# Kernel optimization log

Hardware: AMD Instinct MI355X
Metric: run time of the kernel (lower is better)

Reference implementation:

```python
import jax, jax.numpy as jnp
import numpy as np
import math

# ShiftedL2Loss constants derived from init kwargs
SAMPLE_RATE = 48000
ALPHA = 100.0
MAX_DIST = 1.5
DIST_SAMPLES = int(SAMPLE_RATE * MAX_DIST / 340)  # 211
T_WIN = 2 ** int(math.floor(math.log(DIST_SAMPLES, 2)))  # t = 128
S_SHIFTS = T_WIN * 2 + 1                                  # S = 257
T_BIG = T_WIN + S_SHIFTS - 1                              # T = 384
DT = T_WIN                                                # dT = t


def _blackman_window(M):
    # torch.blackman_window(M, periodic=False)
    n = jnp.arange(M, dtype=jnp.float32)
    denom = jnp.float32(M - 1)
    return (0.42 - 0.5 * jnp.cos(2.0 * jnp.pi * n / denom)
            + 0.08 * jnp.cos(4.0 * jnp.pi * n / denom))


def setup_inputs() -> dict:
    key = jax.random.key(0)
    k1, k2 = jax.random.split(key)
    B, C, L = 4, 8, 15104  # L = 118 * 128 -> exact tiling
    data = jax.random.normal(k1, (B, C, L), dtype=jnp.float32)
    target = jax.random.normal(k2, (B, C, L), dtype=jnp.float32)
    return {"data": data, "target": target}


def reference(data, target):
    t, S = T_WIN, S_SHIFTS
    w = ALPHA * (1.0 - _blackman_window(S))  # (S,)

    # flatten to (BC, L)
    x = data.reshape(-1, data.shape[-1])
    r = target.reshape(-1, target.shape[-1])
    L = x.shape[-1]
    N = (L - t) // DT + 1
    Ltrim = (N - 1) * DT + t
    x = x[:, :Ltrim]
    r = r[:, :Ltrim]

    # magnitude normalization on the center region
    d = x[:, t:-t]
    rc = r[:, t:-t]
    d = d - jnp.mean(d, axis=1, keepdims=True)
    rc = rc - jnp.mean(rc, axis=1, keepdims=True)
    mag_x = jnp.sqrt(jnp.mean(d ** 2, axis=1, keepdims=True))
    mag_r = jnp.sqrt(jnp.mean(rc ** 2, axis=1, keepdims=True))
    mag_min = jnp.minimum(mag_x, mag_r)
    mag_norm = jnp.sqrt(mag_min * mag_r) + 0.001  # (BC, 1)
    x = x / mag_norm
    r = r / mag_norm

    # zero-pad reference by t on both sides
    r_pad = jnp.pad(r, ((0, 0), (t, t)))  # (BC, Ltrim + 2t)

    # non-overlapping predicted windows: (BC, N, t)
    xw = x.reshape(-1, N, t)

    # shifted reference windows: (BC, N, S, t)
    starts = (jnp.arange(N) * DT)[:, None, None]
    idx = starts + jnp.arange(S)[None, :, None] + jnp.arange(t)[None, None, :]
    yw = r_pad[:, idx]  # gather -> (BC, N, S, t)

    # per-shift MSE over the window: (BC, N, S)
    mse = jnp.mean((xw[:, :, None, :] - yw) ** 2, axis=-1)

    # shift-weighted penalty, min over shifts, mean over everything
    loss = (mse + 1.0) * (w[None, None, :] + 1.0) - 1.0
    loss = jnp.amin(loss, axis=-1)  # (BC, N)
    return jnp.mean(loss).reshape(1)
```

## Files before the change

### kernel.cpp

```cpp
#include <hip/hip_runtime.h>
#include <math.h>

#define ROWS 32
#define LROW 15104
#define TWIN 128
#define SSH  257
#define NWIN 118
#define TRIM 14848
#define NW   (ROWS * NWIN)
#define NBLK (NW / 4)
#define SEGS 8
#define SEGLEN (TRIM / SEGS)
#define NSEG4 (SEGLEN / 4)


__global__ __launch_bounds__(256) void stats_partial(
        const float* __restrict__ data,
        const float* __restrict__ target,
        float4* __restrict__ partials) {
    int blk = blockIdx.x;
    int row = blk >> 3;
    int seg = blk & 7;
    int tid = threadIdx.x;

    const float4* x4 = (const float4*)(data   + row * LROW + TWIN + seg * SEGLEN);
    const float4* r4 = (const float4*)(target + row * LROW + TWIN + seg * SEGLEN);
    float sd = 0.f, sd2 = 0.f, sr = 0.f, sr2 = 0.f;
    for (int i = tid; i < NSEG4; i += 256) {
        float4 a = x4[i], b = r4[i];
        sd  += a.x + a.y + a.z + a.w;
        sd2 += a.x*a.x + a.y*a.y + a.z*a.z + a.w*a.w;
        sr  += b.x + b.y + b.z + b.w;
        sr2 += b.x*b.x + b.y*b.y + b.z*b.z + b.w*b.w;
    }
    __shared__ float sh[4][256];
    sh[0][tid] = sd; sh[1][tid] = sd2; sh[2][tid] = sr; sh[3][tid] = sr2;
    __syncthreads();
    for (int off = 128; off > 0; off >>= 1) {
        if (tid < off) {
            sh[0][tid] += sh[0][tid + off];
            sh[1][tid] += sh[1][tid + off];
            sh[2][tid] += sh[2][tid + off];
            sh[3][tid] += sh[3][tid + off];
        }
        __syncthreads();
    }
    if (tid == 0)
        partials[blk] = make_float4(sh[0][0], sh[1][0], sh[2][0], sh[3][0]);
}

__global__ __launch_bounds__(256) void loss_kernel(
        const float* __restrict__ data,
        const float* __restrict__ target,
        const float4* __restrict__ partials,
        float* __restrict__ blocksums) {
    int tid  = threadIdx.x;
    int wave = tid >> 6;
    int lane = tid & 63;
    int widx = blockIdx.x * 4 + wave;
    int row  = widx / NWIN;
    int n    = widx % NWIN;

    float scale;
    {
        const float4* pr = partials + row * SEGS;
        float sd = 0.f, sd2 = 0.f, sr = 0.f, sr2 = 0.f;
        #pragma unroll
        for (int i = 0; i < SEGS; ++i) {
            float4 p = pr[i];
            sd += p.x; sd2 += p.y; sr += p.z; sr2 += p.w;
        }
        const float inv = 1.0f / (float)TRIM;
        float md = sd * inv, mr = sr * inv;
        float vx = fmaxf(sd2 * inv - md * md, 0.f);
        float vr = fmaxf(sr2 * inv - mr * mr, 0.f);
        float mag_x = sqrtf(vx), mag_r = sqrtf(vr);
        float mag_min = fminf(mag_x, mag_r);
        scale = 1.0f / (sqrtf(mag_min * mag_r) + 0.001f);
    }

    __shared__ float xs[4][TWIN];
    __shared__ float ys[4][3 * TWIN];

    const float* xr = data   + row * LROW + n * TWIN;
    const float* rr = target + row * LROW;
    int base = n * TWIN;

    {
        float2 v = *(const float2*)(xr + 2 * lane);
        xs[wave][2 * lane]     = v.x * scale;
        xs[wave][2 * lane + 1] = v.y * scale;
    }
    for (int j = lane; j < 96; j += 64) {
        int g0 = base + 4 * j - TWIN;
        float4 v = make_float4(0.f, 0.f, 0.f, 0.f);
        if (g0 >= 0 && g0 < LROW) v = *(const float4*)(rr + g0);
        *(float4*)&ys[wave][4 * j] =
            make_float4(v.x * scale, v.y * scale, v.z * scale, v.w * scale);
    }

    float sx, part;
    {
        float xa = xs[wave][lane], xb = xs[wave][lane + 64];
        float ya = ys[wave][256 + lane], yb = ys[wave][320 + lane];
        float d1 = xa - ya, d2 = xb - yb;
        part = d1 * d1 + d2 * d2;
        sx   = xa * xa + xb * xb;
        #pragma unroll
        for (int off = 32; off > 0; off >>= 1) {
            part += __shfl_xor(part, off, 64);
            sx   += __shfl_xor(sx,   off, 64);
        }
    }

    const float4* xs4 = (const float4*)xs[wave];
    const float4* ys4 = (const float4*)ys[wave];

    float4 yv0 = ys4[lane];
    float yf0 = yv0.x, yf1 = yv0.y, yf2 = yv0.z;
    float c0 = 0.f, c1 = 0.f, c2 = 0.f, c3 = 0.f;
    float q = 0.f;

    #pragma unroll
    for (int kb = 0; kb < 32; ++kb) {
        float4 xv  = xs4[kb];
        float4 yv1 = ys4[lane + kb + 1];
        c0 += xv.x*yv0.x + xv.y*yv0.y + xv.z*yv0.z + xv.w*yv0.w;
        c1 += xv.x*yv0.y + xv.y*yv0.z + xv.z*yv0.w + xv.w*yv1.x;
        c2 += xv.x*yv0.z + xv.y*yv0.w + xv.z*yv1.x + xv.w*yv1.y;
        c3 += xv.x*yv0.w + xv.y*yv1.x + xv.z*yv1.y + xv.w*yv1.z;
        q  += yv0.x*yv0.x + yv0.y*yv0.y + yv0.z*yv0.z + yv0.w*yv0.w;
        yv0 = yv1;
    }
    float sy0 = q;
    float sy1 = sy0 - yf0*yf0 + yv0.x*yv0.x;
    float sy2 = sy1 - yf1*yf1 + yv0.y*yv0.y;
    float sy3 = sy2 - yf2*yf2 + yv0.z*yv0.z;

    const float inv = 1.0f / (float)TWIN;
    int   s0  = lane * 4;
    float lmin = 1e30f;
    {
        float mse, ph, cp, bw, w;
        mse = (sx - 2.f*c0 + sy0) * inv;
        ph  = (float)(s0 + 0) * (float)(M_PI / 128.0);
        cp  = __cosf(ph); bw = 0.42f - 0.5f*cp + 0.08f*(2.f*cp*cp - 1.f);
        w   = 100.f * (1.f - bw);
        lmin = fminf(lmin, (mse + 1.f) * (w + 1.f) - 1.f);
        mse = (sx - 2.f*c1 + sy1) * inv;
        ph  = (float)(s0 + 1) * (float)(M_PI / 128.0);
        cp  = __cosf(ph); bw = 0.42f - 0.5f*cp + 0.08f*(2.f*cp*cp - 1.f);
        w   = 100.f * (1.f - bw);
        lmin = fminf(lmin, (mse + 1.f) * (w + 1.f) - 1.f);
        mse = (sx - 2.f*c2 + sy2) * inv;
        ph  = (float)(s0 + 2) * (float)(M_PI / 128.0);
        cp  = __cosf(ph); bw = 0.42f - 0.5f*cp + 0.08f*(2.f*cp*cp - 1.f);
        w   = 100.f * (1.f - bw);
        lmin = fminf(lmin, (mse + 1.f) * (w + 1.f) - 1.f);
        mse = (sx - 2.f*c3 + sy3) * inv;
        ph  = (float)(s0 + 3) * (float)(M_PI / 128.0);
        cp  = __cosf(ph); bw = 0.42f - 0.5f*cp + 0.08f*(2.f*cp*cp - 1.f);
        w   = 100.f * (1.f - bw);
        lmin = fminf(lmin, (mse + 1.f) * (w + 1.f) - 1.f);
    }

    {
        float mse256 = part * inv;
        float l256 = (mse256 + 1.f) * 101.f - 1.f;
        lmin = fminf(lmin, l256);
    }
    #pragma unroll
    for (int off = 32; off > 0; off >>= 1)
        lmin = fminf(lmin, __shfl_xor(lmin, off, 64));

    __shared__ float wl[4];
    if (lane == 0) wl[wave] = lmin;
    __syncthreads();
    if (tid == 0) {
        blocksums[blockIdx.x] =
            ((wl[0] + wl[1]) + (wl[2] + wl[3]));
    }
}

__global__ __launch_bounds__(256) void finish_kernel(
        const float* __restrict__ blocksums,
        float* __restrict__ out) {
    int tid = threadIdx.x;
    float s = 0.f;
    for (int i = tid; i < NBLK; i += 256) s += blocksums[i];
    __shared__ float sh[256];
    sh[tid] = s;
    __syncthreads();
    for (int off = 128; off > 0; off >>= 1) {
        if (tid < off) sh[tid] += sh[tid + off];
        __syncthreads();
    }
    if (tid == 0) out[0] = sh[0] / (float)NW;
}

extern "C" void kernel_launch(void* const* d_in, const int* in_sizes, int n_in,
                              void* d_out, int out_size, void* d_ws, size_t ws_size,
                              hipStream_t stream) {
    const float* data   = (const float*)d_in[0];
    const float* target = (const float*)d_in[1];
    float4* partials  = (float4*)d_ws;
    float*  blocksums = (float*)((char*)d_ws + 8192);

    stats_partial<<<ROWS * SEGS, 256, 0, stream>>>(data, target, partials);
    loss_kernel<<<NBLK, 256, 0, stream>>>(data, target, partials, blocksums);
    finish_kernel<<<1, 256, 0, stream>>>(blocksums, (float*)d_out);
}
```

Before: 19.54 us.

## Fuse row statistics into loss kernel with 8-window blocks sharing reference panel

Removes the separate statistics kernel: each block recomputes the full-row mean and energy sums before scaling its windows. Blocks now process eight consecutive windows with a shared reference panel, and a block index swizzle spreads work across dies. This saves a kernel launch and the dependency between launches, at the cost of every block redundantly reading the whole row (mostly from L2).

Measured after the change: 18.39 us. -5.9%, faster.

```diff
diff --git a/kernel.cpp b/kernel.cpp
--- a/kernel.cpp
+++ b/kernel.cpp
@@ -4,70 +4,62 @@
 #define ROWS 32
 #define LROW 15104
 #define TWIN 128
-#define SSH  257
 #define NWIN 118
 #define TRIM 14848
 #define NW   (ROWS * NWIN)
-#define NBLK (NW / 4)
-#define SEGS 8
-#define SEGLEN (TRIM / SEGS)
-#define NSEG4 (SEGLEN / 4)
-
-
-__global__ __launch_bounds__(256) void stats_partial(
+#define WPB  8
+#define BPR  15
+#define NBLK (ROWS * BPR)
+#define XPAN (WPB * TWIN)
+#define YPAN ((WPB + 3) * TWIN)
+
+__global__ __launch_bounds__(512) void loss_fused(
         const float* __restrict__ data,
         const float* __restrict__ target,
-        float4* __restrict__ partials) {
-    int blk = blockIdx.x;
-    int row = blk >> 3;
-    int seg = blk & 7;
-    int tid = threadIdx.x;
-
-    const float4* x4 = (const float4*)(data   + row * LROW + TWIN + seg * SEGLEN);
-    const float4* r4 = (const float4*)(target + row * LROW + TWIN + seg * SEGLEN);
-    float sd = 0.f, sd2 = 0.f, sr = 0.f, sr2 = 0.f;
-    for (int i = tid; i < NSEG4; i += 256) {
-        float4 a = x4[i], b = r4[i];
-        sd  += a.x + a.y + a.z + a.w;
-        sd2 += a.x*a.x + a.y*a.y + a.z*a.z + a.w*a.w;
-        sr  += b.x + b.y + b.z + b.w;
-        sr2 += b.x*b.x + b.y*b.y + b.z*b.z + b.w*b.w;
-    }
-    __shared__ float sh[4][256];
-    sh[0][tid] = sd; sh[1][tid] = sd2; sh[2][tid] = sr; sh[3][tid] = sr2;
-    __syncthreads();
-    for (int off = 128; off > 0; off >>= 1) {
-        if (tid < off) {
-            sh[0][tid] += sh[0][tid + off];
-            sh[1][tid] += sh[1][tid + off];
-            sh[2][tid] += sh[2][tid + off];
-            sh[3][tid] += sh[3][tid + off];
-        }
-        __syncthreads();
-    }
-    if (tid == 0)
-        partials[blk] = make_float4(sh[0][0], sh[1][0], sh[2][0], sh[3][0]);
-}
-
-__global__ __launch_bounds__(256) void loss_kernel(
-        const float* __restrict__ data,
-        const float* __restrict__ target,
-        const float4* __restrict__ partials,
         float* __restrict__ blocksums) {
+    int b0 = blockIdx.x;
+    int b  = (b0 & 7) * (NBLK / 8) + (b0 >> 3);
+    int row = b / BPR;
+    int n0  = (b % BPR) * WPB;
     int tid  = threadIdx.x;
     int wave = tid >> 6;
     int lane = tid & 63;
-    int widx = blockIdx.x * 4 + wave;
-    int row  = widx / NWIN;
-    int n    = widx % NWIN;
-
-    float scale;
+
+    __shared__ float xs[XPAN];
+    __shared__ float ys[YPAN];
+    __shared__ float4 wsum[8];
+    __shared__ float s_scale;
+    __shared__ float wl[8];
+
+    const float* xrow = data   + row * LROW;
+    const float* rrow = target + row * LROW;
+
     {
-        const float4* pr = partials + row * SEGS;
+        const float4* x4 = (const float4*)(xrow + TWIN);
+        const float4* r4 = (const float4*)(rrow + TWIN);
         float sd = 0.f, sd2 = 0.f, sr = 0.f, sr2 = 0.f;
-        #pragma unroll
-        for (int i = 0; i < SEGS; ++i) {
-            float4 p = pr[i];
+        for (int i = tid; i < TRIM / 4; i += 512) {
+            float4 a = x4[i], bv = r4[i];
+            sd  += a.x + a.y + a.z + a.w;
+            sd2 += a.x*a.x + a.y*a.y + a.z*a.z + a.w*a.w;
+            sr  += bv.x + bv.y + bv.z + bv.w;
+            sr2 += bv.x*bv.x + bv.y*bv.y + bv.z*bv.z + bv.w*bv.w;
+        }
+        #pragma unroll
+        for (int off = 32; off > 0; off >>= 1) {
+            sd  += __shfl_xor(sd,  off, 64);
+            sd2 += __shfl_xor(sd2, off, 64);
+            sr  += __shfl_xor(sr,  off, 64);
+            sr2 += __shfl_xor(sr2, off, 64);
+        }
+        if (lane == 0) wsum[wave] = make_float4(sd, sd2, sr, sr2);
+    }
+    __syncthreads();
+    if (tid == 0) {
+        float sd = 0.f, sd2 = 0.f, sr = 0.f, sr2 = 0.f;
+        #pragma unroll
+        for (int i = 0; i < 8; ++i) {
+            float4 p = wsum[i];
             sd += p.x; sd2 += p.y; sr += p.z; sr2 += p.w;
         }
         const float inv = 1.0f / (float)TRIM;
@@ -76,109 +68,113 @@
         float vr = fmaxf(sr2 * inv - mr * mr, 0.f);
         float mag_x = sqrtf(vx), mag_r = sqrtf(vr);
         float mag_min = fminf(mag_x, mag_r);
-        scale = 1.0f / (sqrtf(mag_min * mag_r) + 0.001f);
-    }
-
-    __shared__ float xs[4][TWIN];
-    __shared__ float ys[4][3 * TWIN];
-
-    const float* xr = data   + row * LROW + n * TWIN;
-    const float* rr = target + row * LROW;
-    int base = n * TWIN;
-
-    {
-        float2 v = *(const float2*)(xr + 2 * lane);
-        xs[wave][2 * lane]     = v.x * scale;
-        xs[wave][2 * lane + 1] = v.y * scale;
-    }
-    for (int j = lane; j < 96; j += 64) {
-        int g0 = base + 4 * j - TWIN;
+        s_scale = 1.0f / (sqrtf(mag_min * mag_r) + 0.001f);
+    }
+    __syncthreads();
+    float scale = s_scale;
+
+    for (int j = tid; j < XPAN / 4; j += 512) {
+        int g = n0 * TWIN + 4 * j;
         float4 v = make_float4(0.f, 0.f, 0.f, 0.f);
-        if (g0 >= 0 && g0 < LROW) v = *(const float4*)(rr + g0);
-        *(float4*)&ys[wave][4 * j] =
+        if (g < LROW) v = *(const float4*)(xrow + g);
+        *(float4*)&xs[4 * j] =
             make_float4(v.x * scale, v.y * scale, v.z * scale, v.w * scale);
     }
-
-    float sx, part;
-    {
-        float xa = xs[wave][lane], xb = xs[wave][lane + 64];
-        float ya = ys[wave][256 + lane], yb = ys[wave][320 + lane];
-        float d1 = xa - ya, d2 = xb - yb;
-        part = d1 * d1 + d2 * d2;
-        sx   = xa * xa + xb * xb;
-        #pragma unroll
-        for (int off = 32; off > 0; off >>= 1) {
-            part += __shfl_xor(part, off, 64);
-            sx   += __shfl_xor(sx,   off, 64);
-        }
-    }
-
-    const float4* xs4 = (const float4*)xs[wave];
-    const float4* ys4 = (const float4*)ys[wave];
-
-    float4 yv0 = ys4[lane];
-    float yf0 = yv0.x, yf1 = yv0.y, yf2 = yv0.z;
-    float c0 = 0.f, c1 = 0.f, c2 = 0.f, c3 = 0.f;
-    float q = 0.f;
-
-    #pragma unroll
-    for (int kb = 0; kb < 32; ++kb) {
-        float4 xv  = xs4[kb];
-        float4 yv1 = ys4[lane + kb + 1];
-        c0 += xv.x*yv0.x + xv.y*yv0.y + xv.z*yv0.z + xv.w*yv0.w;
-        c1 += xv.x*yv0.y + xv.y*yv0.z + xv.z*yv0.w + xv.w*yv1.x;
-        c2 += xv.x*yv0.z + xv.y*yv0.w + xv.z*yv1.x + xv.w*yv1.y;
-        c3 += xv.x*yv0.w + xv.y*yv1.x + xv.z*yv1.y + xv.w*yv1.z;
-        q  += yv0.x*yv0.x + yv0.y*yv0.y + yv0.z*yv0.z + yv0.w*yv0.w;
-        yv0 = yv1;
-    }
-    float sy0 = q;
-    float sy1 = sy0 - yf0*yf0 + yv0.x*yv0.x;
-    float sy2 = sy1 - yf1*yf1 + yv0.y*yv0.y;
-    float sy3 = sy2 - yf2*yf2 + yv0.z*yv0.z;
-
-    const float inv = 1.0f / (float)TWIN;
-    int   s0  = lane * 4;
-    float lmin = 1e30f;
-    {
-        float mse, ph, cp, bw, w;
-        mse = (sx - 2.f*c0 + sy0) * inv;
-        ph  = (float)(s0 + 0) * (float)(M_PI / 128.0);
-        cp  = __cosf(ph); bw = 0.42f - 0.5f*cp + 0.08f*(2.f*cp*cp - 1.f);
-        w   = 100.f * (1.f - bw);
-        lmin = fminf(lmin, (mse + 1.f) * (w + 1.f) - 1.f);
-        mse = (sx - 2.f*c1 + sy1) * inv;
-        ph  = (float)(s0 + 1) * (float)(M_PI / 128.0);
-        cp  = __cosf(ph); bw = 0.42f - 0.5f*cp + 0.08f*(2.f*cp*cp - 1.f);
-        w   = 100.f * (1.f - bw);
-        lmin = fminf(lmin, (mse + 1.f) * (w + 1.f) - 1.f);
-        mse = (sx - 2.f*c2 + sy2) * inv;
-        ph  = (float)(s0 + 2) * (float)(M_PI / 128.0);
-        cp  = __cosf(ph); bw = 0.42f - 0.5f*cp + 0.08f*(2.f*cp*cp - 1.f);
-        w   = 100.f * (1.f - bw);
-        lmin = fminf(lmin, (mse + 1.f) * (w + 1.f) - 1.f);
-        mse = (sx - 2.f*c3 + sy3) * inv;
-        ph  = (float)(s0 + 3) * (float)(M_PI / 128.0);
-        cp  = __cosf(ph); bw = 0.42f - 0.5f*cp + 0.08f*(2.f*cp*cp - 1.f);
-        w   = 100.f * (1.f - bw);
-        lmin = fminf(lmin, (mse + 1.f) * (w + 1.f) - 1.f);
-    }
-
-    {
-        float mse256 = part * inv;
-        float l256 = (mse256 + 1.f) * 101.f - 1.f;
-        lmin = fminf(lmin, l256);
-    }
-    #pragma unroll
-    for (int off = 32; off > 0; off >>= 1)
-        lmin = fminf(lmin, __shfl_xor(lmin, off, 64));
-
-    __shared__ float wl[4];
+    for (int j = tid; j < YPAN / 4; j += 512) {
+        int g = (n0 - 1) * TWIN + 4 * j;
+        float4 v = make_float4(0.f, 0.f, 0.f, 0.f);
+        if (g >= 0 && g < LROW) v = *(const float4*)(rrow + g);
+        *(float4*)&ys[4 * j] =
+            make_float4(v.x * scale, v.y * scale, v.z * scale, v.w * scale);
+    }
+    __syncthreads();
+
+    int n = n0 + wave;
+    float lmin = 0.f;
+    if (n < NWIN) {
+        const float* xw = xs + wave * TWIN;
+        const float* yw = ys + wave * TWIN;
+
+        float sx, part;
+        {
+            float xa = xw[lane], xb = xw[lane + 64];
+            float ya = yw[256 + lane], yb = yw[320 + lane];
+            float d1 = xa - ya, d2 = xb - yb;
+            part = d1 * d1 + d2 * d2;
+            sx   = xa * xa + xb * xb;
+            #pragma unroll
+            for (int off = 32; off > 0; off >>= 1) {
+                part += __shfl_xor(part, off, 64);
+                sx   += __shfl_xor(sx,   off, 64);
+            }
+        }
+
+        const float4* xs4 = (const float4*)xw;
+        const float4* ys4 = (const float4*)yw;
+
+        float4 yv0 = ys4[lane];
+        float yf0 = yv0.x, yf1 = yv0.y, yf2 = yv0.z;
+        float c0 = 0.f, c1 = 0.f, c2 = 0.f, c3 = 0.f;
+        float q = 0.f;
+
+        #pragma unroll
+        for (int kb = 0; kb < 32; ++kb) {
+            float4 xv  = xs4[kb];
+            float4 yv1 = ys4[lane + kb + 1];
+            c0 += xv.x*yv0.x + xv.y*yv0.y + xv.z*yv0.z + xv.w*yv0.w;
+            c1 += xv.x*yv0.y + xv.y*yv0.z + xv.z*yv0.w + xv.w*yv1.x;
+            c2 += xv.x*yv0.z + xv.y*yv0.w + xv.z*yv1.x + xv.w*yv1.y;
+            c3 += xv.x*yv0.w + xv.y*yv1.x + xv.z*yv1.y + xv.w*yv1.z;
+            q  += yv0.x*yv0.x + yv0.y*yv0.y + yv0.z*yv0.z + yv0.w*yv0.w;
+            yv0 = yv1;
+        }
+        float sy0 = q;
+        float sy1 = sy0 - yf0*yf0 + yv0.x*yv0.x;
+        float sy2 = sy1 - yf1*yf1 + yv0.y*yv0.y;
+        float sy3 = sy2 - yf2*yf2 + yv0.z*yv0.z;
+
+        const float inv = 1.0f / (float)TWIN;
+        int   s0  = lane * 4;
+        lmin = 1e30f;
+        {
+            float mse, ph, cp, bw, w;
+            mse = (sx - 2.f*c0 + sy0) * inv;
+            ph  = (float)(s0 + 0) * (float)(M_PI / 128.0);
+            cp  = __cosf(ph); bw = 0.42f - 0.5f*cp + 0.08f*(2.f*cp*cp - 1.f);
+            w   = 100.f * (1.f - bw);
+            lmin = fminf(lmin, (mse + 1.f) * (w + 1.f) - 1.f);
+            mse = (sx - 2.f*c1 + sy1) * inv;
+            ph  = (float)(s0 + 1) * (float)(M_PI / 128.0);
+            cp  = __cosf(ph); bw = 0.42f - 0.5f*cp + 0.08f*(2.f*cp*cp - 1.f);
+            w   = 100.f * (1.f - bw);
+            lmin = fminf(lmin, (mse + 1.f) * (w + 1.f) - 1.f);
+            mse = (sx - 2.f*c2 + sy2) * inv;
+            ph  = (float)(s0 + 2) * (float)(M_PI / 128.0);
+            cp  = __cosf(ph); bw = 0.42f - 0.5f*cp + 0.08f*(2.f*cp*cp - 1.f);
+            w   = 100.f * (1.f - bw);
+            lmin = fminf(lmin, (mse + 1.f) * (w + 1.f) - 1.f);
+            mse = (sx - 2.f*c3 + sy3) * inv;
+            ph  = (float)(s0 + 3) * (float)(M_PI / 128.0);
+            cp  = __cosf(ph); bw = 0.42f - 0.5f*cp + 0.08f*(2.f*cp*cp - 1.f);
+            w   = 100.f * (1.f - bw);
+            lmin = fminf(lmin, (mse + 1.f) * (w + 1.f) - 1.f);
+        }
+        {
+            float mse256 = part * inv;
+            lmin = fminf(lmin, (mse256 + 1.f) * 101.f - 1.f);
+        }
+        #pragma unroll
+        for (int off = 32; off > 0; off >>= 1)
+            lmin = fminf(lmin, __shfl_xor(lmin, off, 64));
+    }
+
     if (lane == 0) wl[wave] = lmin;
     __syncthreads();
     if (tid == 0) {
-        blocksums[blockIdx.x] =
-            ((wl[0] + wl[1]) + (wl[2] + wl[3]));
+        float s = 0.f;
+        #pragma unroll
+        for (int i = 0; i < 8; ++i) s += wl[i];
+        blocksums[b] = s;
     }
 }
 
@@ -203,10 +199,8 @@
                               hipStream_t stream) {
     const float* data   = (const float*)d_in[0];
     const float* target = (const float*)d_in[1];
-    float4* partials  = (float4*)d_ws;
-    float*  blocksums = (float*)((char*)d_ws + 8192);
-
-    stats_partial<<<ROWS * SEGS, 256, 0, stream>>>(data, target, partials);
-    loss_kernel<<<NBLK, 256, 0, stream>>>(data, target, partials, blocksums);
+    float* blocksums = (float*)d_ws;
+
+    loss_fused<<<NBLK, 512, 0, stream>>>(data, target, blocksums);
     finish_kernel<<<1, 256, 0, stream>>>(blocksums, (float*)d_out);
 }
```
